# Kernel optimization log

Measured on AMD Instinct MI355X. Metric: run time of the kernel, lower is better.

The kernel has to match this reference:

```python
import jax, jax.numpy as jnp
import numpy as np

N_PATCH = 80
N_FFT = 160
PAD = N_FFT // 2 - N_PATCH // 2  # 40
D = 64       # n_delays
NC = 512     # candidate TFs
L = 0.0064   # physical patch size (m)
DX = 4e-05   # pixel size (m)
FWHM = 0.0015


def setup_inputs() -> dict:
    key = jax.random.key(0)
    k0, k1 = jax.random.split(key)
    patch_stack = jax.random.normal(k0, (1, D, N_PATCH, N_PATCH), jnp.float32)
    # Fourier coordinates (centered grid), as in get_fourier_coord(N=160, l=0.0064)
    f = np.fft.fftshift(np.fft.fftfreq(N_FFT, d=L / N_FFT)) * 2 * np.pi
    KX, KY = np.meshgrid(f, f, indexing='xy')
    k_rad = np.sqrt(KX ** 2 + KY ** 2)
    k2D = jnp.asarray(k_rad, jnp.float32)
    theta2D = jnp.asarray(np.arctan2(KY, KX), jnp.float32)
    # self.k: ifftshifted radial wavenumber, broadcast shape [1,1,160,160]
    k_loss = jnp.asarray(np.fft.ifftshift(k_rad), jnp.float32)[None, None]
    # Gaussian apodization window, sigma = fwhm/4e-5/sqrt(2 ln 2)
    sigma = FWHM / DX / np.sqrt(2.0 * np.log(2.0))
    c = np.arange(N_PATCH) - (N_PATCH - 1) / 2.0
    gx, gy = np.meshgrid(c, c)
    gaussian_window = jnp.asarray(
        np.exp(-(gx ** 2 + gy ** 2) / (2.0 * sigma ** 2)), jnp.float32)[None]
    delays = jnp.linspace(-5e-5, 5e-5, D).astype(jnp.float32)
    # candidate (dc, x, y) wavefront parameters
    cand_params = (jax.random.uniform(k1, (NC, 3), jnp.float32, -1.0, 1.0)
                   * jnp.array([1e-5, 5e-6, 5e-6], jnp.float32))
    return dict(patch_stack=patch_stack, gaussian_window=gaussian_window,
                delays=delays, k2D=k2D, theta2D=theta2D, k_loss=k_loss,
                cand_params=cand_params)


def reference(patch_stack, gaussian_window, delays, k2D, theta2D, k_loss, cand_params):
    n = patch_stack.shape[-1]
    pad = n // 2
    # window, zero-pad to double size, ifftshift, FFT2 -> Y [1, D, 2n, 2n]
    yw = patch_stack * gaussian_window
    ypad = jnp.pad(yw, ((0, 0), (0, 0), (pad, pad), (pad, pad)))
    Y = jnp.fft.fft2(jnp.fft.ifftshift(ypad, axes=(-2, -1)))
    Yabs_k = jnp.abs(Y) * k_loss

    def make_tf(p):
        dc, x, y = p[0], p[1], p[2]
        w = dc + x * jnp.cos(2.0 * theta2D) + y * jnp.sin(2.0 * theta2D)
        # (exp(-i k d) + exp(i k d)) / 2 == cos(k d)  (real-valued TF)
        phase = k2D[None] * (delays[:, None, None] - w[None])  # [D, 2n, 2n]
        return jnp.fft.ifftshift(jnp.cos(phase), axes=(-2, -1))[None]  # [1, D, 2n, 2n]

    def step(carry, p):
        best_loss, best_X, best_idx, idx = carry
        H = make_tf(p)
        rhs = jnp.sum(Y * H, axis=-3, keepdims=True)   # conj(H) == H (real)
        lhs = jnp.sum(H * H, axis=-3, keepdims=True)   # |H|^2
        X = rhs / lhs                                   # [1, 1, 2n, 2n] complex
        loss = jnp.mean((Yabs_k - jnp.abs(H * X) * k_loss) ** 2,
                        axis=(-3, -2, -1))[0]
        better = loss < best_loss
        carry = (jnp.where(better, loss, best_loss),
                 jnp.where(better, X, best_X),
                 jnp.where(better, idx, best_idx),
                 idx + 1)
        return carry, None

    init = (jnp.array(jnp.inf, jnp.float32),
            jnp.zeros((1, 1, 2 * n, 2 * n), jnp.complex64),
            jnp.array(0, jnp.int32), jnp.array(0, jnp.int32))
    (best_loss, best_X, best_idx, _), _ = jax.lax.scan(step, init, cand_params)

    img = jnp.fft.fftshift(jnp.fft.ifft2(best_X), axes=(-2, -1))
    best_x = jnp.real(img[..., pad:pad + n, pad:pad + n])  # crop_half
    best_params = cand_params[best_idx]
    return best_x, best_params, best_loss
```

## Files before the change

### kernel.cpp

```cpp
#include <hip/hip_runtime.h>

#define NF 160
#define NP 80
#define ND 64
#define NC 512
#define NV 81
#define NPIXH (NF*NV)
#define NPIXP 13056
#define NXBLK 51
#define NJ NXBLK
#define CPB 16
#define TWO_PI 6.283185307179586f

#define IP_AR 0
#define IP_AI 1
#define IP_BR 2
#define IP_BI 3
#define IP_P  4
#define IP_Q  5
#define IP_R  6
#define IP_C2T 7
#define IP_S2T 8
#define IP_K  9
#define IP_CD0 10
#define IP_SD0 11
#define IP_CD1 12
#define IP_SD1 13
#define IP_TCD 14
#define IP_S0 15
#define IP_W  16
#define NPRM 17

__device__ __forceinline__ void rot(float& c, float& s, float stc, float sts) {
  float t1 = s * sts;
  float t2 = s * stc;
  float cn = fmaf(c, stc, -t1);
  s = fmaf(c, sts, t2);
  c = cn;
}

__device__ __forceinline__ void start_i_pow(int n, float& c, float& s) {
  switch (n & 3) {
    case 0: c = 1.f; s = 0.f; break;
    case 1: c = 0.f; s = 1.f; break;
    case 2: c = -1.f; s = 0.f; break;
    default: c = 0.f; s = -1.f; break;
  }
}

__global__ __launch_bounds__(256) void k_fft_x(const float* __restrict__ patch,
                                               const float* __restrict__ gw,
                                               float2* __restrict__ T) {
  int idx = blockIdx.x * 256 + threadIdx.x;
  int v = idx % NV;
  int a = (idx / NV) % NP;
  int d = idx / (NV * NP);
  float c, s;
  start_i_pow(v, c, s);
  float stc, sts;
  sincosf(-TWO_PI * (float)v / (float)NF, &sts, &stc);
  const float* prow = patch + (size_t)(d * NP + a) * NP;
  const float* grow = gw + a * NP;
  float accR = 0.f, accI = 0.f;
  for (int b = 0; b < NP; ++b) {
    float f = prow[b] * grow[b];
    accR = fmaf(f, c, accR);
    accI = fmaf(f, s, accI);
    rot(c, s, stc, sts);
  }
  T[idx] = make_float2(accR, accI);
}

__global__ __launch_bounds__(256) void k_fft_y(const float2* __restrict__ T,
                                               float2* __restrict__ Y) {
  int idx = blockIdx.x * 256 + threadIdx.x;
  int v = idx % NV;
  int ug = (idx / NV) % 40;
  int d = idx / (NV * 40);
  float c[4], s[4], aR[4], aI[4], stc[4], sts[4];
#pragma unroll
  for (int j = 0; j < 4; ++j) {
    int u = ug * 4 + j;
    start_i_pow(u, c[j], s[j]);
    sincosf(-TWO_PI * (float)u / (float)NF, &sts[j], &stc[j]);
    aR[j] = 0.f; aI[j] = 0.f;
  }
  const float2* Tb = T + (size_t)(d * NP) * NV + v;
  for (int a = 0; a < NP; ++a) {
    float2 t = Tb[(size_t)a * NV];
#pragma unroll
    for (int j = 0; j < 4; ++j) {
      aR[j] = fmaf(t.x, c[j], aR[j]);
      aR[j] = fmaf(-t.y, s[j], aR[j]);
      aI[j] = fmaf(t.x, s[j], aI[j]);
      aI[j] = fmaf(t.y, c[j], aI[j]);
      rot(c[j], s[j], stc[j], sts[j]);
    }
  }
#pragma unroll
  for (int j = 0; j < 4; ++j) {
    int u = ug * 4 + j;
    Y[((size_t)d * NF + u) * NV + v] = make_float2(aR[j], aI[j]);
  }
}

__global__ __launch_bounds__(256) void k_prep(const float2* __restrict__ Y,
                                              const float* __restrict__ delays,
                                              const float* __restrict__ kloss,
                                              const float* __restrict__ theta,
                                              float4* __restrict__ Yk4,
                                              float* __restrict__ prm) {
  int p = blockIdx.x * 256 + threadIdx.x;
  if (p >= NPIXH) {
#pragma unroll
    for (int jj = 0; jj < ND / 4; ++jj)
      Yk4[(size_t)jj * NPIXP + p] = make_float4(0.f, 0.f, 0.f, 0.f);
    prm[IP_AR * NPIXP + p] = 0.f;  prm[IP_AI * NPIXP + p] = 0.f;
    prm[IP_BR * NPIXP + p] = 0.f;  prm[IP_BI * NPIXP + p] = 0.f;
    prm[IP_P * NPIXP + p] = 1.f;   prm[IP_Q * NPIXP + p] = 0.f;
    prm[IP_R * NPIXP + p] = 1.f;   prm[IP_C2T * NPIXP + p] = 0.f;
    prm[IP_S2T * NPIXP + p] = 0.f; prm[IP_K * NPIXP + p] = 0.f;
    prm[IP_CD0 * NPIXP + p] = 1.f; prm[IP_SD0 * NPIXP + p] = 0.f;
    prm[IP_CD1 * NPIXP + p] = 1.f; prm[IP_SD1 * NPIXP + p] = 0.f;
    prm[IP_TCD * NPIXP + p] = 2.f; prm[IP_S0 * NPIXP + p] = 0.f;
    prm[IP_W * NPIXP + p] = 0.f;
    return;
  }
  int u = p / NV, v = p % NV;
  float k = kloss[u * NF + v];
  float th = theta[((u + 80) % NF) * NF + ((v + 80) % NF)];
  float c2t = cosf(2.f * th), s2t = sinf(2.f * th);
  float w;
  if (v == 0 || v == 80) {
    if (u == 0 || u == 80) w = 1.f;
    else if (u < 80) w = 2.f;
    else w = 0.f;
  } else w = 2.f;
  float d0 = delays[0], d1 = delays[1];
  float sd0f, cd0f;
  sincosf(k * d0, &sd0f, &cd0f);
  float stc, sts;
  sincosf(k * (d1 - d0), &sts, &stc);
  float tcd = 2.f * stc;
  float cd = cd0f, sd = sd0f;
  float cd1s = 0.f, sd1s = 0.f;
  float Ar = 0.f, Ai = 0.f, Br = 0.f, Bi = 0.f, Pm = 0.f, Qm = 0.f, Rm = 0.f, S0 = 0.f;
  float yktmp[ND];
#pragma unroll
  for (int d = 0; d < ND; ++d) {
    if (d == 1) { cd1s = cd; sd1s = sd; }
    float2 y = Y[((size_t)d * NF + u) * NV + v];
    Ar = fmaf(y.x, cd, Ar);  Ai = fmaf(y.y, cd, Ai);
    Br = fmaf(y.x, sd, Br);  Bi = fmaf(y.y, sd, Bi);
    Pm = fmaf(cd, cd, Pm);  Qm = fmaf(cd, sd, Qm);  Rm = fmaf(sd, sd, Rm);
    float yk = sqrtf(fmaf(y.x, y.x, y.y * y.y)) * k;
    yktmp[d] = yk;
    S0 = fmaf(yk, yk, S0);
    rot(cd, sd, stc, sts);
  }
#pragma unroll
  for (int jj = 0; jj < ND / 4; ++jj)
    Yk4[(size_t)jj * NPIXP + p] = make_float4(yktmp[2 * jj], yktmp[63 - 2 * jj],
                                              yktmp[2 * jj + 1], yktmp[62 - 2 * jj]);
  prm[IP_AR * NPIXP + p] = Ar;   prm[IP_AI * NPIXP + p] = Ai;
  prm[IP_BR * NPIXP + p] = Br;   prm[IP_BI * NPIXP + p] = Bi;
  prm[IP_P * NPIXP + p] = Pm;    prm[IP_Q * NPIXP + p] = Qm;
  prm[IP_R * NPIXP + p] = Rm;    prm[IP_C2T * NPIXP + p] = c2t;
  prm[IP_S2T * NPIXP + p] = s2t; prm[IP_K * NPIXP + p] = k;
  prm[IP_CD0 * NPIXP + p] = cd0f; prm[IP_SD0 * NPIXP + p] = sd0f;
  prm[IP_CD1 * NPIXP + p] = cd1s; prm[IP_SD1 * NPIXP + p] = sd1s;
  prm[IP_TCD * NPIXP + p] = tcd; prm[IP_S0 * NPIXP + p] = S0;
  prm[IP_W * NPIXP + p] = w;
}

__global__ __launch_bounds__(256, 3) void k_cand(const float4* __restrict__ Yk4,
                                                 const float* __restrict__ prm,
                                                 const float* __restrict__ cand,
                                                 float* __restrict__ partial) {
  int p = blockIdx.x * 256 + threadIdx.x;
  int c0 = blockIdx.y * CPB;
  float Ar = prm[IP_AR * NPIXP + p], Ai = prm[IP_AI * NPIXP + p];
  float Br = prm[IP_BR * NPIXP + p], Bi = prm[IP_BI * NPIXP + p];
  float Pm = prm[IP_P * NPIXP + p], Qm = prm[IP_Q * NPIXP + p], Rm = prm[IP_R * NPIXP + p];
  float c2t = prm[IP_C2T * NPIXP + p], s2t = prm[IP_S2T * NPIXP + p];
  float k = prm[IP_K * NPIXP + p];
  float cd0 = prm[IP_CD0 * NPIXP + p], sd0 = prm[IP_SD0 * NPIXP + p];
  float cd1 = prm[IP_CD1 * NPIXP + p], sd1 = prm[IP_SD1 * NPIXP + p];
  float tcd = prm[IP_TCD * NPIXP + p], S0 = prm[IP_S0 * NPIXP + p];
  float wgt = prm[IP_W * NPIXP + p];
  float4 yk[ND / 4];
#pragma unroll
  for (int jj = 0; jj < ND / 4; ++jj) yk[jj] = Yk4[(size_t)jj * NPIXP + p];
#pragma unroll
  for (int jj = 0; jj < ND / 4; ++jj)
    asm volatile("" : "+v"(yk[jj].x), "+v"(yk[jj].y), "+v"(yk[jj].z), "+v"(yk[jj].w));
  int wid = threadIdx.x >> 6;
  int lane = threadIdx.x & 63;
  __shared__ float sdata[CPB][4];
  for (int ci = 0; ci < CPB; ++ci) {
    int c = c0 + ci;
    float dc = cand[c * 3 + 0], xx = cand[c * 3 + 1], yy = cand[c * 3 + 2];
    float w_ = fmaf(xx, c2t, fmaf(yy, s2t, dc));
    float kw = k * w_;
    float sw, cw;
    __sincosf(kw, &sw, &cw);
    float rr = fmaf(cw, Ar, sw * Br);
    float ri = fmaf(cw, Ai, sw * Bi);
    float lhs = fmaf(cw * cw, Pm, fmaf(2.f * cw * sw, Qm, sw * sw * Rm));
    float rabs = __builtin_amdgcn_sqrtf(fmaf(rr, rr, ri * ri));
    float rl = __builtin_amdgcn_rcpf(lhs);
    float e = fmaf(-lhs, rl, 1.f);
    rl = fmaf(rl, e, rl);
    float kX = k * rabs * rl;
    float t0 = cd0 * cw, u0 = sd0 * sw;
    float t1 = cd1 * cw, u1 = sd1 * sw;
    float Am1 = t0 + u0, Bm1 = t0 - u0;
    float Ac  = t1 + u1, Bc  = t1 - u1;
    float MA0 = yk[0].x * fabsf(Am1);
    float MB0 = yk[0].y * fabsf(Bm1);
    float MA1 = yk[0].z * fabsf(Ac);
    float MB1 = yk[0].w * fabsf(Bc);
#pragma unroll
    for (int jj = 1; jj < ND / 4; ++jj) {
      float An = fmaf(tcd, Ac, -Am1);
      float Bn = fmaf(tcd, Bc, -Bm1);
      MA0 = fmaf(yk[jj].x, fabsf(An), MA0);
      MB0 = fmaf(yk[jj].y, fabsf(Bn), MB0);
      float An2 = fmaf(tcd, An, -Ac);
      float Bn2 = fmaf(tcd, Bn, -Bc);
      MA1 = fmaf(yk[jj].z, fabsf(An2), MA1);
      MB1 = fmaf(yk[jj].w, fabsf(Bn2), MB1);
      Am1 = An; Ac = An2;
      Bm1 = Bn; Bc = Bn2;
    }
    float M = (MA0 + MA1) + (MB0 + MB1);
    float contrib = fmaf(kX * kX, lhs, fmaf(-2.f * kX, M, S0)) * wgt;
    for (int off = 32; off > 0; off >>= 1) contrib += __shfl_xor(contrib, off);
    if (lane == 0) sdata[ci][wid] = contrib;
  }
  __syncthreads();
  if (threadIdx.x < CPB) {
    int ci = threadIdx.x;
    float s = (sdata[ci][0] + sdata[ci][1]) + (sdata[ci][2] + sdata[ci][3]);
    partial[(size_t)blockIdx.x * NC + c0 + ci] = s;
  }
}

__global__ void k_argmin(const float* __restrict__ partial,
                         const float* __restrict__ cand,
                         float* __restrict__ out, int* __restrict__ bestIdx) {
  __shared__ float sl[NC];
  __shared__ int si[NC];
  int c = threadIdx.x;
  float s = 0.f;
#pragma unroll
  for (int j = 0; j < NJ; ++j) s += partial[(size_t)j * NC + c];
  sl[c] = s * (1.f / 1638400.f);
  si[c] = c;
  __syncthreads();
  for (int off = 256; off > 0; off >>= 1) {
    if (c < off) {
      float l2 = sl[c + off]; int i2 = si[c + off];
      if (l2 < sl[c] || (l2 == sl[c] && i2 < si[c])) { sl[c] = l2; si[c] = i2; }
    }
    __syncthreads();
  }
  if (c == 0) {
    int bi = si[0];
    out[6400] = cand[bi * 3 + 0];
    out[6401] = cand[bi * 3 + 1];
    out[6402] = cand[bi * 3 + 2];
    out[6403] = sl[0];
    *bestIdx = bi;
  }
}

__global__ __launch_bounds__(256) void k_ifft_u(const float* __restrict__ prm,
                                                const float* __restrict__ cand,
                                                const int* __restrict__ bestIdx,
                                                float2* __restrict__ G) {
  int u = blockIdx.x;
  __shared__ float xr[NF], xi[NF];
  int bi = *bestIdx;
  float dc = cand[bi * 3 + 0], xx = cand[bi * 3 + 1], yy = cand[bi * 3 + 2];
  int v = threadIdx.x;
  if (v < NF) {
    float sign = 1.f;
    int ph;
    if (v <= 80) {
      ph = u * NV + v;
    } else {
      int u2 = (NF - u) % NF;
      ph = u2 * NV + (NF - v);
      sign = -1.f;
    }
    float Ar = prm[IP_AR * NPIXP + ph], Ai = prm[IP_AI * NPIXP + ph];
    float Br = prm[IP_BR * NPIXP + ph], Bi = prm[IP_BI * NPIXP + ph];
    float Pm = prm[IP_P * NPIXP + ph], Qm = prm[IP_Q * NPIXP + ph], Rm = prm[IP_R * NPIXP + ph];
    float c2t = prm[IP_C2T * NPIXP + ph], s2t = prm[IP_S2T * NPIXP + ph];
    float k = prm[IP_K * NPIXP + ph];
    float w_ = fmaf(xx, c2t, fmaf(yy, s2t, dc));
    float sw, cw;
    sincosf(k * w_, &sw, &cw);
    float rr = fmaf(cw, Ar, sw * Br);
    float ri = fmaf(cw, Ai, sw * Bi);
    float lhs = fmaf(cw * cw, Pm, fmaf(2.f * cw * sw, Qm, sw * sw * Rm));
    xr[v] = rr / lhs;
    xi[v] = sign * ri / lhs;
  }
  __syncthreads();
  int b = threadIdx.x;
  if (b < NP) {
    int xb = (b + 120) % NF;
    float stc, sts;
    sincosf(TWO_PI * (float)xb / (float)NF, &sts, &stc);
    float c = 1.f, s = 0.f, accR = 0.f, accI = 0.f;
    for (int vv = 0; vv < NF; ++vv) {
      float xrv = xr[vv], xiv = xi[vv];
      accR = fmaf(xrv, c, accR); accR = fmaf(-xiv, s, accR);
      accI = fmaf(xrv, s, accI); accI = fmaf(xiv, c, accI);
      rot(c, s, stc, sts);
    }
    G[(size_t)u * NP + b] = make_float2(accR, accI);
  }
}

__global__ __launch_bounds__(64) void k_ifft_y(const float2* __restrict__ G,
                                               float* __restrict__ out) {
  int idx = blockIdx.x * 64 + threadIdx.x;
  int b = idx % NP;
  int a = idx / NP;
  int ya = (a + 120) % NF;
  float stc, sts;
  sincosf(TWO_PI * (float)ya / (float)NF, &sts, &stc);
  float c = 1.f, s = 0.f, accR = 0.f;
  for (int u = 0; u < NF; ++u) {
    float2 g = G[(size_t)u * NP + b];
    accR = fmaf(g.x, c, accR);
    accR = fmaf(-g.y, s, accR);
    rot(c, s, stc, sts);
  }
  out[idx] = accR * (1.f / 25600.f);
}

extern "C" void kernel_launch(void* const* d_in, const int* in_sizes, int n_in,
                              void* d_out, int out_size, void* d_ws, size_t ws_size,
                              hipStream_t stream) {
  (void)in_sizes; (void)n_in; (void)out_size; (void)ws_size;
  const float* patch  = (const float*)d_in[0];
  const float* gw     = (const float*)d_in[1];
  const float* delays = (const float*)d_in[2];
  const float* theta  = (const float*)d_in[4];
  const float* kloss  = (const float*)d_in[5];
  const float* cand   = (const float*)d_in[6];
  float* out = (float*)d_out;

  char* ws = (char*)d_ws;
  size_t off = 0;
  float2* Y = (float2*)(ws + off);      off += (size_t)ND * NF * NV * 8;
  float2* T = (float2*)(ws + off);      off += (size_t)ND * NP * NV * 8;
  float4* Yk4 = (float4*)(ws + off);    off += (size_t)(ND / 4) * NPIXP * 16;
  float* prm = (float*)(ws + off);      off += (size_t)NPRM * NPIXP * 4;
  float* partial = (float*)(ws + off);  off += (size_t)NJ * NC * 4;
  float2* G = (float2*)(ws + off);      off += (size_t)NF * NP * 8;
  int* bestIdx = (int*)(ws + off);

  hipLaunchKernelGGL(k_fft_x, dim3((ND * NP * NV) / 256), dim3(256), 0, stream, patch, gw, T);
  hipLaunchKernelGGL(k_fft_y, dim3((ND * 40 * NV) / 256), dim3(256), 0, stream, T, Y);
  hipLaunchKernelGGL(k_prep, dim3(NXBLK), dim3(256), 0, stream, Y, delays, kloss, theta, Yk4, prm);
  hipLaunchKernelGGL(k_cand, dim3(NXBLK, NC / CPB), dim3(256), 0, stream, Yk4, prm, cand, partial);
  hipLaunchKernelGGL(k_argmin, dim3(1), dim3(NC), 0, stream, partial, cand, out, bestIdx);
  hipLaunchKernelGGL(k_ifft_u, dim3(NF), dim3(256), 0, stream, prm, cand, bestIdx, G);
  hipLaunchKernelGGL(k_ifft_y, dim3(100), dim3(64), 0, stream, G, out);
}
```

Baseline: 100.5 us.

## Fuse all stages into one cooperative persistent kernel with grid syncs

Replaces the seven separate kernel launches with a single cooperative kernel of 256 blocks that loops over each stage's work in grid-stride fashion, separated by grid.sync(). This removes per-launch overhead and inter-kernel gaps. The cost is grid-wide barriers, and occupancy is capped by the register-heavy candidate stage under launch_bounds(256,2). Small stages such as prep (51 blocks) and argmin (1 block) also leave most of the grid idle. Adds unroll pragmas and a two-per-thread argmin reduction.

```diff
diff --git a/kernel.cpp b/kernel.cpp
--- a/kernel.cpp
+++ b/kernel.cpp
@@ -1,4 +1,7 @@
 #include <hip/hip_runtime.h>
+#include <hip/hip_cooperative_groups.h>
+
+namespace cg = cooperative_groups;
 
 #define NF 160
 #define NP 80
@@ -10,6 +13,9 @@
 #define NXBLK 51
 #define NJ NXBLK
 #define CPB 16
+#define NBLK 256
+#define NTHR 256
+#define NTH (NBLK*NTHR)
 #define TWO_PI 6.283185307179586f
 
 #define IP_AR 0
@@ -48,299 +54,314 @@
   }
 }
 
-__global__ __launch_bounds__(256) void k_fft_x(const float* __restrict__ patch,
-                                               const float* __restrict__ gw,
-                                               float2* __restrict__ T) {
-  int idx = blockIdx.x * 256 + threadIdx.x;
-  int v = idx % NV;
-  int a = (idx / NV) % NP;
-  int d = idx / (NV * NP);
-  float c, s;
-  start_i_pow(v, c, s);
-  float stc, sts;
-  sincosf(-TWO_PI * (float)v / (float)NF, &sts, &stc);
-  const float* prow = patch + (size_t)(d * NP + a) * NP;
-  const float* grow = gw + a * NP;
-  float accR = 0.f, accI = 0.f;
-  for (int b = 0; b < NP; ++b) {
-    float f = prow[b] * grow[b];
-    accR = fmaf(f, c, accR);
-    accI = fmaf(f, s, accI);
-    rot(c, s, stc, sts);
-  }
-  T[idx] = make_float2(accR, accI);
-}
-
-__global__ __launch_bounds__(256) void k_fft_y(const float2* __restrict__ T,
-                                               float2* __restrict__ Y) {
-  int idx = blockIdx.x * 256 + threadIdx.x;
-  int v = idx % NV;
-  int ug = (idx / NV) % 40;
-  int d = idx / (NV * 40);
-  float c[4], s[4], aR[4], aI[4], stc[4], sts[4];
-#pragma unroll
-  for (int j = 0; j < 4; ++j) {
-    int u = ug * 4 + j;
-    start_i_pow(u, c[j], s[j]);
-    sincosf(-TWO_PI * (float)u / (float)NF, &sts[j], &stc[j]);
-    aR[j] = 0.f; aI[j] = 0.f;
-  }
-  const float2* Tb = T + (size_t)(d * NP) * NV + v;
-  for (int a = 0; a < NP; ++a) {
-    float2 t = Tb[(size_t)a * NV];
+__global__ __launch_bounds__(256, 2) void k_mega(
+    const float* __restrict__ patch, const float* __restrict__ gw,
+    const float* __restrict__ delays, const float* __restrict__ kloss,
+    const float* __restrict__ theta, const float* __restrict__ cand,
+    float* __restrict__ out,
+    float2* __restrict__ T, float2* __restrict__ Y,
+    float4* __restrict__ Yk4, float* __restrict__ prm,
+    float* __restrict__ partial, float2* __restrict__ G,
+    int* __restrict__ bestIdx) {
+  cg::grid_group grid = cg::this_grid();
+  const int tid = blockIdx.x * NTHR + threadIdx.x;
+
+  for (int idx = tid; idx < ND * NP * NV; idx += NTH) {
+    int v = idx % NV;
+    int a = (idx / NV) % NP;
+    int d = idx / (NV * NP);
+    float c, s;
+    start_i_pow(v, c, s);
+    float stc, sts;
+    sincosf(-TWO_PI * (float)v / (float)NF, &sts, &stc);
+    const float* prow = patch + (size_t)(d * NP + a) * NP;
+    const float* grow = gw + a * NP;
+    float accR = 0.f, accI = 0.f;
+#pragma unroll 4
+    for (int b = 0; b < NP; ++b) {
+      float f = prow[b] * grow[b];
+      accR = fmaf(f, c, accR);
+      accI = fmaf(f, s, accI);
+      rot(c, s, stc, sts);
+    }
+    T[idx] = make_float2(accR, accI);
+  }
+  grid.sync();
+
+  for (int idx = tid; idx < ND * 40 * NV; idx += NTH) {
+    int v = idx % NV;
+    int ug = (idx / NV) % 40;
+    int d = idx / (NV * 40);
+    float c[4], s[4], aR[4], aI[4], stc[4], sts[4];
 #pragma unroll
     for (int j = 0; j < 4; ++j) {
-      aR[j] = fmaf(t.x, c[j], aR[j]);
-      aR[j] = fmaf(-t.y, s[j], aR[j]);
-      aI[j] = fmaf(t.x, s[j], aI[j]);
-      aI[j] = fmaf(t.y, c[j], aI[j]);
-      rot(c[j], s[j], stc[j], sts[j]);
-    }
-  }
-#pragma unroll
-  for (int j = 0; j < 4; ++j) {
-    int u = ug * 4 + j;
-    Y[((size_t)d * NF + u) * NV + v] = make_float2(aR[j], aI[j]);
-  }
-}
-
-__global__ __launch_bounds__(256) void k_prep(const float2* __restrict__ Y,
-                                              const float* __restrict__ delays,
-                                              const float* __restrict__ kloss,
-                                              const float* __restrict__ theta,
-                                              float4* __restrict__ Yk4,
-                                              float* __restrict__ prm) {
-  int p = blockIdx.x * 256 + threadIdx.x;
-  if (p >= NPIXH) {
+      int u = ug * 4 + j;
+      start_i_pow(u, c[j], s[j]);
+      sincosf(-TWO_PI * (float)u / (float)NF, &sts[j], &stc[j]);
+      aR[j] = 0.f; aI[j] = 0.f;
+    }
+    const float2* Tb = T + (size_t)(d * NP) * NV + v;
+#pragma unroll 4
+    for (int a = 0; a < NP; ++a) {
+      float2 t = Tb[(size_t)a * NV];
+#pragma unroll
+      for (int j = 0; j < 4; ++j) {
+        aR[j] = fmaf(t.x, c[j], aR[j]);
+        aR[j] = fmaf(-t.y, s[j], aR[j]);
+        aI[j] = fmaf(t.x, s[j], aI[j]);
+        aI[j] = fmaf(t.y, c[j], aI[j]);
+        rot(c[j], s[j], stc[j], sts[j]);
+      }
+    }
+#pragma unroll
+    for (int j = 0; j < 4; ++j) {
+      int u = ug * 4 + j;
+      Y[((size_t)d * NF + u) * NV + v] = make_float2(aR[j], aI[j]);
+    }
+  }
+  grid.sync();
+
+  for (int p = tid; p < NPIXP; p += NTH) {
+    if (p >= NPIXH) {
+#pragma unroll
+      for (int jj = 0; jj < ND / 4; ++jj)
+        Yk4[(size_t)jj * NPIXP + p] = make_float4(0.f, 0.f, 0.f, 0.f);
+      prm[IP_AR * NPIXP + p] = 0.f;  prm[IP_AI * NPIXP + p] = 0.f;
+      prm[IP_BR * NPIXP + p] = 0.f;  prm[IP_BI * NPIXP + p] = 0.f;
+      prm[IP_P * NPIXP + p] = 1.f;   prm[IP_Q * NPIXP + p] = 0.f;
+      prm[IP_R * NPIXP + p] = 1.f;   prm[IP_C2T * NPIXP + p] = 0.f;
+      prm[IP_S2T * NPIXP + p] = 0.f; prm[IP_K * NPIXP + p] = 0.f;
+      prm[IP_CD0 * NPIXP + p] = 1.f; prm[IP_SD0 * NPIXP + p] = 0.f;
+      prm[IP_CD1 * NPIXP + p] = 1.f; prm[IP_SD1 * NPIXP + p] = 0.f;
+      prm[IP_TCD * NPIXP + p] = 2.f; prm[IP_S0 * NPIXP + p] = 0.f;
+      prm[IP_W * NPIXP + p] = 0.f;
+      continue;
+    }
+    int u = p / NV, v = p % NV;
+    float k = kloss[u * NF + v];
+    float th = theta[((u + 80) % NF) * NF + ((v + 80) % NF)];
+    float c2t = cosf(2.f * th), s2t = sinf(2.f * th);
+    float w;
+    if (v == 0 || v == 80) {
+      if (u == 0 || u == 80) w = 1.f;
+      else if (u < 80) w = 2.f;
+      else w = 0.f;
+    } else w = 2.f;
+    float d0 = delays[0], d1 = delays[1];
+    float sd0f, cd0f;
+    sincosf(k * d0, &sd0f, &cd0f);
+    float stc, sts;
+    sincosf(k * (d1 - d0), &sts, &stc);
+    float tcd = 2.f * stc;
+    float cd = cd0f, sd = sd0f;
+    float cd1s = 0.f, sd1s = 0.f;
+    float Ar = 0.f, Ai = 0.f, Br = 0.f, Bi = 0.f, Pm = 0.f, Qm = 0.f, Rm = 0.f, S0 = 0.f;
+    float yktmp[ND];
+#pragma unroll
+    for (int d = 0; d < ND; ++d) {
+      if (d == 1) { cd1s = cd; sd1s = sd; }
+      float2 y = Y[((size_t)d * NF + u) * NV + v];
+      Ar = fmaf(y.x, cd, Ar);  Ai = fmaf(y.y, cd, Ai);
+      Br = fmaf(y.x, sd, Br);  Bi = fmaf(y.y, sd, Bi);
+      Pm = fmaf(cd, cd, Pm);  Qm = fmaf(cd, sd, Qm);  Rm = fmaf(sd, sd, Rm);
+      float yk = sqrtf(fmaf(y.x, y.x, y.y * y.y)) * k;
+      yktmp[d] = yk;
+      S0 = fmaf(yk, yk, S0);
+      rot(cd, sd, stc, sts);
+    }
 #pragma unroll
     for (int jj = 0; jj < ND / 4; ++jj)
-      Yk4[(size_t)jj * NPIXP + p] = make_float4(0.f, 0.f, 0.f, 0.f);
-    prm[IP_AR * NPIXP + p] = 0.f;  prm[IP_AI * NPIXP + p] = 0.f;
-    prm[IP_BR * NPIXP + p] = 0.f;  prm[IP_BI * NPIXP + p] = 0.f;
-    prm[IP_P * NPIXP + p] = 1.f;   prm[IP_Q * NPIXP + p] = 0.f;
-    prm[IP_R * NPIXP + p] = 1.f;   prm[IP_C2T * NPIXP + p] = 0.f;
-    prm[IP_S2T * NPIXP + p] = 0.f; prm[IP_K * NPIXP + p] = 0.f;
-    prm[IP_CD0 * NPIXP + p] = 1.f; prm[IP_SD0 * NPIXP + p] = 0.f;
-    prm[IP_CD1 * NPIXP + p] = 1.f; prm[IP_SD1 * NPIXP + p] = 0.f;
-    prm[IP_TCD * NPIXP + p] = 2.f; prm[IP_S0 * NPIXP + p] = 0.f;
-    prm[IP_W * NPIXP + p] = 0.f;
-    return;
-  }
-  int u = p / NV, v = p % NV;
-  float k = kloss[u * NF + v];
-  float th = theta[((u + 80) % NF) * NF + ((v + 80) % NF)];
-  float c2t = cosf(2.f * th), s2t = sinf(2.f * th);
-  float w;
-  if (v == 0 || v == 80) {
-    if (u == 0 || u == 80) w = 1.f;
-    else if (u < 80) w = 2.f;
-    else w = 0.f;
-  } else w = 2.f;
-  float d0 = delays[0], d1 = delays[1];
-  float sd0f, cd0f;
-  sincosf(k * d0, &sd0f, &cd0f);
-  float stc, sts;
-  sincosf(k * (d1 - d0), &sts, &stc);
-  float tcd = 2.f * stc;
-  float cd = cd0f, sd = sd0f;
-  float cd1s = 0.f, sd1s = 0.f;
-  float Ar = 0.f, Ai = 0.f, Br = 0.f, Bi = 0.f, Pm = 0.f, Qm = 0.f, Rm = 0.f, S0 = 0.f;
-  float yktmp[ND];
-#pragma unroll
-  for (int d = 0; d < ND; ++d) {
-    if (d == 1) { cd1s = cd; sd1s = sd; }
-    float2 y = Y[((size_t)d * NF + u) * NV + v];
-    Ar = fmaf(y.x, cd, Ar);  Ai = fmaf(y.y, cd, Ai);
-    Br = fmaf(y.x, sd, Br);  Bi = fmaf(y.y, sd, Bi);
-    Pm = fmaf(cd, cd, Pm);  Qm = fmaf(cd, sd, Qm);  Rm = fmaf(sd, sd, Rm);
-    float yk = sqrtf(fmaf(y.x, y.x, y.y * y.y)) * k;
-    yktmp[d] = yk;
-    S0 = fmaf(yk, yk, S0);
-    rot(cd, sd, stc, sts);
-  }
-#pragma unroll
-  for (int jj = 0; jj < ND / 4; ++jj)
-    Yk4[(size_t)jj * NPIXP + p] = make_float4(yktmp[2 * jj], yktmp[63 - 2 * jj],
-                                              yktmp[2 * jj + 1], yktmp[62 - 2 * jj]);
-  prm[IP_AR * NPIXP + p] = Ar;   prm[IP_AI * NPIXP + p] = Ai;
-  prm[IP_BR * NPIXP + p] = Br;   prm[IP_BI * NPIXP + p] = Bi;
-  prm[IP_P * NPIXP + p] = Pm;    prm[IP_Q * NPIXP + p] = Qm;
-  prm[IP_R * NPIXP + p] = Rm;    prm[IP_C2T * NPIXP + p] = c2t;
-  prm[IP_S2T * NPIXP + p] = s2t; prm[IP_K * NPIXP + p] = k;
-  prm[IP_CD0 * NPIXP + p] = cd0f; prm[IP_SD0 * NPIXP + p] = sd0f;
-  prm[IP_CD1 * NPIXP + p] = cd1s; prm[IP_SD1 * NPIXP + p] = sd1s;
-  prm[IP_TCD * NPIXP + p] = tcd; prm[IP_S0 * NPIXP + p] = S0;
-  prm[IP_W * NPIXP + p] = w;
-}
-
-__global__ __launch_bounds__(256, 3) void k_cand(const float4* __restrict__ Yk4,
-                                                 const float* __restrict__ prm,
-                                                 const float* __restrict__ cand,
-                                                 float* __restrict__ partial) {
-  int p = blockIdx.x * 256 + threadIdx.x;
-  int c0 = blockIdx.y * CPB;
-  float Ar = prm[IP_AR * NPIXP + p], Ai = prm[IP_AI * NPIXP + p];
-  float Br = prm[IP_BR * NPIXP + p], Bi = prm[IP_BI * NPIXP + p];
-  float Pm = prm[IP_P * NPIXP + p], Qm = prm[IP_Q * NPIXP + p], Rm = prm[IP_R * NPIXP + p];
-  float c2t = prm[IP_C2T * NPIXP + p], s2t = prm[IP_S2T * NPIXP + p];
-  float k = prm[IP_K * NPIXP + p];
-  float cd0 = prm[IP_CD0 * NPIXP + p], sd0 = prm[IP_SD0 * NPIXP + p];
-  float cd1 = prm[IP_CD1 * NPIXP + p], sd1 = prm[IP_SD1 * NPIXP + p];
-  float tcd = prm[IP_TCD * NPIXP + p], S0 = prm[IP_S0 * NPIXP + p];
-  float wgt = prm[IP_W * NPIXP + p];
-  float4 yk[ND / 4];
-#pragma unroll
-  for (int jj = 0; jj < ND / 4; ++jj) yk[jj] = Yk4[(size_t)jj * NPIXP + p];
-#pragma unroll
-  for (int jj = 0; jj < ND / 4; ++jj)
-    asm volatile("" : "+v"(yk[jj].x), "+v"(yk[jj].y), "+v"(yk[jj].z), "+v"(yk[jj].w));
-  int wid = threadIdx.x >> 6;
-  int lane = threadIdx.x & 63;
-  __shared__ float sdata[CPB][4];
-  for (int ci = 0; ci < CPB; ++ci) {
-    int c = c0 + ci;
-    float dc = cand[c * 3 + 0], xx = cand[c * 3 + 1], yy = cand[c * 3 + 2];
-    float w_ = fmaf(xx, c2t, fmaf(yy, s2t, dc));
-    float kw = k * w_;
-    float sw, cw;
-    __sincosf(kw, &sw, &cw);
-    float rr = fmaf(cw, Ar, sw * Br);
-    float ri = fmaf(cw, Ai, sw * Bi);
-    float lhs = fmaf(cw * cw, Pm, fmaf(2.f * cw * sw, Qm, sw * sw * Rm));
-    float rabs = __builtin_amdgcn_sqrtf(fmaf(rr, rr, ri * ri));
-    float rl = __builtin_amdgcn_rcpf(lhs);
-    float e = fmaf(-lhs, rl, 1.f);
-    rl = fmaf(rl, e, rl);
-    float kX = k * rabs * rl;
-    float t0 = cd0 * cw, u0 = sd0 * sw;
-    float t1 = cd1 * cw, u1 = sd1 * sw;
-    float Am1 = t0 + u0, Bm1 = t0 - u0;
-    float Ac  = t1 + u1, Bc  = t1 - u1;
-    float MA0 = yk[0].x * fabsf(Am1);
-    float MB0 = yk[0].y * fabsf(Bm1);
-    float MA1 = yk[0].z * fabsf(Ac);
-    float MB1 = yk[0].w * fabsf(Bc);
-#pragma unroll
-    for (int jj = 1; jj < ND / 4; ++jj) {
-      float An = fmaf(tcd, Ac, -Am1);
-      float Bn = fmaf(tcd, Bc, -Bm1);
-      MA0 = fmaf(yk[jj].x, fabsf(An), MA0);
-      MB0 = fmaf(yk[jj].y, fabsf(Bn), MB0);
-      float An2 = fmaf(tcd, An, -Ac);
-      float Bn2 = fmaf(tcd, Bn, -Bc);
-      MA1 = fmaf(yk[jj].z, fabsf(An2), MA1);
-      MB1 = fmaf(yk[jj].w, fabsf(Bn2), MB1);
-      Am1 = An; Ac = An2;
-      Bm1 = Bn; Bc = Bn2;
-    }
-    float M = (MA0 + MA1) + (MB0 + MB1);
-    float contrib = fmaf(kX * kX, lhs, fmaf(-2.f * kX, M, S0)) * wgt;
-    for (int off = 32; off > 0; off >>= 1) contrib += __shfl_xor(contrib, off);
-    if (lane == 0) sdata[ci][wid] = contrib;
-  }
-  __syncthreads();
-  if (threadIdx.x < CPB) {
-    int ci = threadIdx.x;
-    float s = (sdata[ci][0] + sdata[ci][1]) + (sdata[ci][2] + sdata[ci][3]);
-    partial[(size_t)blockIdx.x * NC + c0 + ci] = s;
-  }
-}
-
-__global__ void k_argmin(const float* __restrict__ partial,
-                         const float* __restrict__ cand,
-                         float* __restrict__ out, int* __restrict__ bestIdx) {
-  __shared__ float sl[NC];
-  __shared__ int si[NC];
-  int c = threadIdx.x;
-  float s = 0.f;
-#pragma unroll
-  for (int j = 0; j < NJ; ++j) s += partial[(size_t)j * NC + c];
-  sl[c] = s * (1.f / 1638400.f);
-  si[c] = c;
-  __syncthreads();
-  for (int off = 256; off > 0; off >>= 1) {
-    if (c < off) {
-      float l2 = sl[c + off]; int i2 = si[c + off];
-      if (l2 < sl[c] || (l2 == sl[c] && i2 < si[c])) { sl[c] = l2; si[c] = i2; }
-    }
+      Yk4[(size_t)jj * NPIXP + p] = make_float4(yktmp[2 * jj], yktmp[63 - 2 * jj],
+                                                yktmp[2 * jj + 1], yktmp[62 - 2 * jj]);
+    prm[IP_AR * NPIXP + p] = Ar;   prm[IP_AI * NPIXP + p] = Ai;
+    prm[IP_BR * NPIXP + p] = Br;   prm[IP_BI * NPIXP + p] = Bi;
+    prm[IP_P * NPIXP + p] = Pm;    prm[IP_Q * NPIXP + p] = Qm;
+    prm[IP_R * NPIXP + p] = Rm;    prm[IP_C2T * NPIXP + p] = c2t;
+    prm[IP_S2T * NPIXP + p] = s2t; prm[IP_K * NPIXP + p] = k;
+    prm[IP_CD0 * NPIXP + p] = cd0f; prm[IP_SD0 * NPIXP + p] = sd0f;
+    prm[IP_CD1 * NPIXP + p] = cd1s; prm[IP_SD1 * NPIXP + p] = sd1s;
+    prm[IP_TCD * NPIXP + p] = tcd; prm[IP_S0 * NPIXP + p] = S0;
+    prm[IP_W * NPIXP + p] = w;
+  }
+  grid.sync();
+
+  {
+    int wid = threadIdx.x >> 6;
+    int lane = threadIdx.x & 63;
+    __shared__ float sdata[CPB][4];
+    for (int vb = blockIdx.x; vb < NXBLK * (NC / CPB); vb += NBLK) {
+      int bx = vb % NXBLK;
+      int by = vb / NXBLK;
+      int p = bx * 256 + threadIdx.x;
+      int c0 = by * CPB;
+      float Ar = prm[IP_AR * NPIXP + p], Ai = prm[IP_AI * NPIXP + p];
+      float Br = prm[IP_BR * NPIXP + p], Bi = prm[IP_BI * NPIXP + p];
+      float Pm = prm[IP_P * NPIXP + p], Qm = prm[IP_Q * NPIXP + p], Rm = prm[IP_R * NPIXP + p];
+      float c2t = prm[IP_C2T * NPIXP + p], s2t = prm[IP_S2T * NPIXP + p];
+      float k = prm[IP_K * NPIXP + p];
+      float cd0 = prm[IP_CD0 * NPIXP + p], sd0 = prm[IP_SD0 * NPIXP + p];
+      float cd1 = prm[IP_CD1 * NPIXP + p], sd1 = prm[IP_SD1 * NPIXP + p];
+      float tcd = prm[IP_TCD * NPIXP + p], S0 = prm[IP_S0 * NPIXP + p];
+      float wgt = prm[IP_W * NPIXP + p];
+      float4 yk[ND / 4];
+#pragma unroll
+      for (int jj = 0; jj < ND / 4; ++jj) yk[jj] = Yk4[(size_t)jj * NPIXP + p];
+#pragma unroll
+      for (int jj = 0; jj < ND / 4; ++jj)
+        asm volatile("" : "+v"(yk[jj].x), "+v"(yk[jj].y), "+v"(yk[jj].z), "+v"(yk[jj].w));
+      for (int ci = 0; ci < CPB; ++ci) {
+        int c = c0 + ci;
+        float dc = cand[c * 3 + 0], xx = cand[c * 3 + 1], yy = cand[c * 3 + 2];
+        float w_ = fmaf(xx, c2t, fmaf(yy, s2t, dc));
+        float kw = k * w_;
+        float sw, cw;
+        __sincosf(kw, &sw, &cw);
+        float rr = fmaf(cw, Ar, sw * Br);
+        float ri = fmaf(cw, Ai, sw * Bi);
+        float lhs = fmaf(cw * cw, Pm, fmaf(2.f * cw * sw, Qm, sw * sw * Rm));
+        float rabs = __builtin_amdgcn_sqrtf(fmaf(rr, rr, ri * ri));
+        float rl = __builtin_amdgcn_rcpf(lhs);
+        float e = fmaf(-lhs, rl, 1.f);
+        rl = fmaf(rl, e, rl);
+        float kX = k * rabs * rl;
+        float t0 = cd0 * cw, u0 = sd0 * sw;
+        float t1 = cd1 * cw, u1 = sd1 * sw;
+        float Am1 = t0 + u0, Bm1 = t0 - u0;
+        float Ac  = t1 + u1, Bc  = t1 - u1;
+        float MA0 = yk[0].x * fabsf(Am1);
+        float MB0 = yk[0].y * fabsf(Bm1);
+        float MA1 = yk[0].z * fabsf(Ac);
+        float MB1 = yk[0].w * fabsf(Bc);
+#pragma unroll
+        for (int jj = 1; jj < ND / 4; ++jj) {
+          float An = fmaf(tcd, Ac, -Am1);
+          float Bn = fmaf(tcd, Bc, -Bm1);
+          MA0 = fmaf(yk[jj].x, fabsf(An), MA0);
+          MB0 = fmaf(yk[jj].y, fabsf(Bn), MB0);
+          float An2 = fmaf(tcd, An, -Ac);
+          float Bn2 = fmaf(tcd, Bn, -Bc);
+          MA1 = fmaf(yk[jj].z, fabsf(An2), MA1);
+          MB1 = fmaf(yk[jj].w, fabsf(Bn2), MB1);
+          Am1 = An; Ac = An2;
+          Bm1 = Bn; Bc = Bn2;
+        }
+        float M = (MA0 + MA1) + (MB0 + MB1);
+        float contrib = fmaf(kX * kX, lhs, fmaf(-2.f * kX, M, S0)) * wgt;
+        for (int off = 32; off > 0; off >>= 1) contrib += __shfl_xor(contrib, off);
+        if (lane == 0) sdata[ci][wid] = contrib;
+      }
+      __syncthreads();
+      if (threadIdx.x < CPB) {
+        int ci = threadIdx.x;
+        float s = (sdata[ci][0] + sdata[ci][1]) + (sdata[ci][2] + sdata[ci][3]);
+        partial[(size_t)bx * NC + c0 + ci] = s;
+      }
+      __syncthreads();
+    }
+  }
+  grid.sync();
+
+  if (blockIdx.x == 0) {
+    __shared__ float sl[NTHR];
+    __shared__ int si[NTHR];
+    int c1 = threadIdx.x, c2 = threadIdx.x + NTHR;
+    float s1 = 0.f, s2 = 0.f;
+#pragma unroll
+    for (int j = 0; j < NJ; ++j) {
+      s1 += partial[(size_t)j * NC + c1];
+      s2 += partial[(size_t)j * NC + c2];
+    }
+    float l; int i;
+    if (s2 < s1) { l = s2; i = c2; } else { l = s1; i = c1; }
+    sl[threadIdx.x] = l; si[threadIdx.x] = i;
     __syncthreads();
-  }
-  if (c == 0) {
-    int bi = si[0];
-    out[6400] = cand[bi * 3 + 0];
-    out[6401] = cand[bi * 3 + 1];
-    out[6402] = cand[bi * 3 + 2];
-    out[6403] = sl[0];
-    *bestIdx = bi;
-  }
-}
-
-__global__ __launch_bounds__(256) void k_ifft_u(const float* __restrict__ prm,
-                                                const float* __restrict__ cand,
-                                                const int* __restrict__ bestIdx,
-                                                float2* __restrict__ G) {
-  int u = blockIdx.x;
-  __shared__ float xr[NF], xi[NF];
-  int bi = *bestIdx;
-  float dc = cand[bi * 3 + 0], xx = cand[bi * 3 + 1], yy = cand[bi * 3 + 2];
-  int v = threadIdx.x;
-  if (v < NF) {
-    float sign = 1.f;
-    int ph;
-    if (v <= 80) {
-      ph = u * NV + v;
-    } else {
-      int u2 = (NF - u) % NF;
-      ph = u2 * NV + (NF - v);
-      sign = -1.f;
-    }
-    float Ar = prm[IP_AR * NPIXP + ph], Ai = prm[IP_AI * NPIXP + ph];
-    float Br = prm[IP_BR * NPIXP + ph], Bi = prm[IP_BI * NPIXP + ph];
-    float Pm = prm[IP_P * NPIXP + ph], Qm = prm[IP_Q * NPIXP + ph], Rm = prm[IP_R * NPIXP + ph];
-    float c2t = prm[IP_C2T * NPIXP + ph], s2t = prm[IP_S2T * NPIXP + ph];
-    float k = prm[IP_K * NPIXP + ph];
-    float w_ = fmaf(xx, c2t, fmaf(yy, s2t, dc));
-    float sw, cw;
-    sincosf(k * w_, &sw, &cw);
-    float rr = fmaf(cw, Ar, sw * Br);
-    float ri = fmaf(cw, Ai, sw * Bi);
-    float lhs = fmaf(cw * cw, Pm, fmaf(2.f * cw * sw, Qm, sw * sw * Rm));
-    xr[v] = rr / lhs;
-    xi[v] = sign * ri / lhs;
-  }
-  __syncthreads();
-  int b = threadIdx.x;
-  if (b < NP) {
-    int xb = (b + 120) % NF;
+    for (int off = 128; off > 0; off >>= 1) {
+      if (threadIdx.x < off) {
+        float l2 = sl[threadIdx.x + off]; int i2 = si[threadIdx.x + off];
+        if (l2 < sl[threadIdx.x] || (l2 == sl[threadIdx.x] && i2 < si[threadIdx.x])) {
+          sl[threadIdx.x] = l2; si[threadIdx.x] = i2;
+        }
+      }
+      __syncthreads();
+    }
+    if (threadIdx.x == 0) {
+      int bi = si[0];
+      out[6400] = cand[bi * 3 + 0];
+      out[6401] = cand[bi * 3 + 1];
+      out[6402] = cand[bi * 3 + 2];
+      out[6403] = sl[0] * (1.f / 1638400.f);
+      *bestIdx = bi;
+    }
+  }
+  grid.sync();
+
+  {
+    __shared__ float xr[NF], xi[NF];
+    if (blockIdx.x < NF) {
+      int u = blockIdx.x;
+      int bi = *bestIdx;
+      float dc = cand[bi * 3 + 0], xx = cand[bi * 3 + 1], yy = cand[bi * 3 + 2];
+      int v = threadIdx.x;
+      if (v < NF) {
+        float sign = 1.f;
+        int ph;
+        if (v <= 80) {
+          ph = u * NV + v;
+        } else {
+          int u2 = (NF - u) % NF;
+          ph = u2 * NV + (NF - v);
+          sign = -1.f;
+        }
+        float Ar = prm[IP_AR * NPIXP + ph], Ai = prm[IP_AI * NPIXP + ph];
+        float Br = prm[IP_BR * NPIXP + ph], Bi = prm[IP_BI * NPIXP + ph];
+        float Pm = prm[IP_P * NPIXP + ph], Qm = prm[IP_Q * NPIXP + ph], Rm = prm[IP_R * NPIXP + ph];
+        float c2t = prm[IP_C2T * NPIXP + ph], s2t = prm[IP_S2T * NPIXP + ph];
+        float k = prm[IP_K * NPIXP + ph];
+        float w_ = fmaf(xx, c2t, fmaf(yy, s2t, dc));
+        float sw, cw;
+        sincosf(k * w_, &sw, &cw);
+        float rr = fmaf(cw, Ar, sw * Br);
+        float ri = fmaf(cw, Ai, sw * Bi);
+        float lhs = fmaf(cw * cw, Pm, fmaf(2.f * cw * sw, Qm, sw * sw * Rm));
+        xr[v] = rr / lhs;
+        xi[v] = sign * ri / lhs;
+      }
+      __syncthreads();
+      int b = threadIdx.x;
+      if (b < NP) {
+        int xb = (b + 120) % NF;
+        float stc, sts;
+        sincosf(TWO_PI * (float)xb / (float)NF, &sts, &stc);
+        float c = 1.f, s = 0.f, accR = 0.f, accI = 0.f;
+#pragma unroll 4
+        for (int vv = 0; vv < NF; ++vv) {
+          float xrv = xr[vv], xiv = xi[vv];
+          accR = fmaf(xrv, c, accR); accR = fmaf(-xiv, s, accR);
+          accI = fmaf(xrv, s, accI); accI = fmaf(xiv, c, accI);
+          rot(c, s, stc, sts);
+        }
+        G[(size_t)u * NP + b] = make_float2(accR, accI);
+      }
+    }
+  }
+  grid.sync();
+
+  for (int idx = tid; idx < NP * NP; idx += NTH) {
+    int b = idx % NP;
+    int a = idx / NP;
+    int ya = (a + 120) % NF;
     float stc, sts;
-    sincosf(TWO_PI * (float)xb / (float)NF, &sts, &stc);
-    float c = 1.f, s = 0.f, accR = 0.f, accI = 0.f;
-    for (int vv = 0; vv < NF; ++vv) {
-      float xrv = xr[vv], xiv = xi[vv];
-      accR = fmaf(xrv, c, accR); accR = fmaf(-xiv, s, accR);
-      accI = fmaf(xrv, s, accI); accI = fmaf(xiv, c, accI);
+    sincosf(TWO_PI * (float)ya / (float)NF, &sts, &stc);
+    float c = 1.f, s = 0.f, accR = 0.f;
+#pragma unroll 4
+    for (int u = 0; u < NF; ++u) {
+      float2 g = G[(size_t)u * NP + b];
+      accR = fmaf(g.x, c, accR);
+      accR = fmaf(-g.y, s, accR);
       rot(c, s, stc, sts);
     }
-    G[(size_t)u * NP + b] = make_float2(accR, accI);
-  }
-}
-
-__global__ __launch_bounds__(64) void k_ifft_y(const float2* __restrict__ G,
-                                               float* __restrict__ out) {
-  int idx = blockIdx.x * 64 + threadIdx.x;
-  int b = idx % NP;
-  int a = idx / NP;
-  int ya = (a + 120) % NF;
-  float stc, sts;
-  sincosf(TWO_PI * (float)ya / (float)NF, &sts, &stc);
-  float c = 1.f, s = 0.f, accR = 0.f;
-  for (int u = 0; u < NF; ++u) {
-    float2 g = G[(size_t)u * NP + b];
-    accR = fmaf(g.x, c, accR);
-    accR = fmaf(-g.y, s, accR);
-    rot(c, s, stc, sts);
-  }
-  out[idx] = accR * (1.f / 25600.f);
+    out[idx] = accR * (1.f / 25600.f);
+  }
 }
 
 extern "C" void kernel_launch(void* const* d_in, const int* in_sizes, int n_in,
@@ -365,11 +386,11 @@
   float2* G = (float2*)(ws + off);      off += (size_t)NF * NP * 8;
   int* bestIdx = (int*)(ws + off);
 
-  hipLaunchKernelGGL(k_fft_x, dim3((ND * NP * NV) / 256), dim3(256), 0, stream, patch, gw, T);
-  hipLaunchKernelGGL(k_fft_y, dim3((ND * 40 * NV) / 256), dim3(256), 0, stream, T, Y);
-  hipLaunchKernelGGL(k_prep, dim3(NXBLK), dim3(256), 0, stream, Y, delays, kloss, theta, Yk4, prm);
-  hipLaunchKernelGGL(k_cand, dim3(NXBLK, NC / CPB), dim3(256), 0, stream, Yk4, prm, cand, partial);
-  hipLaunchKernelGGL(k_argmin, dim3(1), dim3(NC), 0, stream, partial, cand, out, bestIdx);
-  hipLaunchKernelGGL(k_ifft_u, dim3(NF), dim3(256), 0, stream, prm, cand, bestIdx, G);
-  hipLaunchKernelGGL(k_ifft_y, dim3(100), dim3(64), 0, stream, G, out);
+  void* args[] = {
+    (void*)&patch, (void*)&gw, (void*)&delays, (void*)&kloss, (void*)&theta,
+    (void*)&cand, (void*)&out, (void*)&T, (void*)&Y, (void*)&Yk4,
+    (void*)&prm, (void*)&partial, (void*)&G, (void*)&bestIdx
+  };
+  hipLaunchCooperativeKernel((const void*)k_mega, dim3(NBLK), dim3(NTHR),
+                             args, 0, stream);
 }
```

Measured after the change: 346.3 us. +244.5%, slower.
